# Performance work log

Hardware: AMD Instinct MI355X
Metric: run time of the kernel (lower is better)

The kernel has to match this reference:

```python
import jax, jax.numpy as jnp
import numpy as np

B, T, D = 2, 2048, 1024
N_HEADS, D_HEAD, WINDOW = 16, 64, 256
SCALE = D_HEAD ** -0.5


def setup_inputs() -> dict:
    key = jax.random.key(0)
    k1, k2, k3 = jax.random.split(key, 3)
    x = jax.random.normal(k1, (B, T, D), dtype=jnp.float32)
    # torch Linear weights are [out_features, in_features], init std=0.02
    w_qkv = jax.random.normal(k2, (3 * N_HEADS * D_HEAD, D), dtype=jnp.float32) * 0.02
    w_out = jax.random.normal(k3, (D, N_HEADS * D_HEAD), dtype=jnp.float32) * 0.02
    return {"x": x, "w_qkv": w_qkv, "w_out": w_out}


def reference(x, w_qkv, w_out):
    b, t, d = x.shape
    qkv = jnp.einsum('btd,ed->bte', x, w_qkv)  # [B,T,3*H*Dh]
    q, k, v = jnp.split(qkv, 3, axis=-1)
    def heads(u):
        return u.reshape(b, t, N_HEADS, D_HEAD).transpose(0, 2, 1, 3)  # [B,H,T,Dh]
    q, k, v = heads(q), heads(k), heads(v)
    scores = jnp.einsum('bhqd,bhkd->bhqk', q, k) * SCALE  # [B,H,T,T]
    pos = jnp.arange(t)
    dist = pos[:, None] - pos[None, :]  # query - key
    allowed = (dist >= 0) & (dist < WINDOW)  # causal sliding window
    neg_inf = jnp.asarray(-jnp.inf, dtype=scores.dtype)
    scores = jnp.where(allowed[None, None], scores, neg_inf)
    attn = jax.nn.softmax(scores, axis=-1)
    out = jnp.einsum('bhqk,bhkd->bhqd', attn, v)  # [B,H,T,Dh]
    out = out.transpose(0, 2, 1, 3).reshape(b, t, N_HEADS * D_HEAD)
    return jnp.einsum('bte,de->btd', out, w_out)
```

## Files before the change

kernel.cpp:

```cpp
#include <hip/hip_runtime.h>
#include <hip/hip_bf16.h>

typedef unsigned short bfu;
typedef __attribute__((ext_vector_type(8))) short short8;
typedef __attribute__((ext_vector_type(4))) float floatx4;

#define B_ 2
#define T_ 2048
#define D_ 1024
#define NH 16
#define DH 64
#define WIN 256
#define QKV_COLS 3072
#define NX  (B_ * T_ * D_)
#define NWQ (QKV_COLS * D_)
#define NWO (D_ * D_)

__device__ __forceinline__ bfu f2b_bits(float f) {
  union { __hip_bfloat16 h; bfu u; } cv;
  cv.h = __float2bfloat16(f);
  return cv.u;
}

__device__ __forceinline__ void gl_lds16(const bfu* g, bfu* l) {
  __builtin_amdgcn_global_load_lds(
      (const __attribute__((address_space(1))) unsigned int*)g,
      (__attribute__((address_space(3))) unsigned int*)l, 16, 0, 0);
}

__global__ void cvt3_kernel(const float* __restrict__ x, const float* __restrict__ wq,
                            const float* __restrict__ wo, bfu* __restrict__ out) {
  int i = (blockIdx.x * 256 + threadIdx.x) * 4;
  const float* src;
  int off;
  if (i < NX)            { src = x;  off = 0; }
  else if (i < NX + NWQ) { src = wq; off = NX; }
  else                   { src = wo; off = NX + NWQ; }
  floatx4 v = *(const floatx4*)(src + (i - off));
  out[i + 0] = f2b_bits(v.x);
  out[i + 1] = f2b_bits(v.y);
  out[i + 2] = f2b_bits(v.z);
  out[i + 3] = f2b_bits(v.w);
}

template <bool OUT_BF16, int TN, bool SCALE_Q>
__global__ __launch_bounds__(256) void gemm_bt_kernel(const bfu* __restrict__ A,
                                                      const bfu* __restrict__ Bm,
                                                      void* __restrict__ C,
                                                      int M, int N, int K) {
  constexpr int NJ = TN / 32;
  __shared__ __align__(16) bfu As[128][64];
  __shared__ __align__(16) bfu Bs[TN][64];
  const int tid = threadIdx.x;
  const int wave = tid >> 6, lane = tid & 63;
  const int quad = lane >> 4, cl = lane & 15;
  const int lr = lane >> 3, lg = lane & 7, sg = lg ^ lr;
  const int wm = (wave >> 1) * 64, wn = (wave & 1) * (TN / 2);
  const int m0 = blockIdx.y * 128, n0 = blockIdx.x * TN;

  floatx4 acc[4][NJ] = {};

  for (int k0 = 0; k0 < K; k0 += 64) {
    __syncthreads();
#pragma unroll
    for (int i = 0; i < 4; ++i) {
      const int row = i * 32 + wave * 8;
      gl_lds16(A + (size_t)(m0 + row + lr) * K + k0 + sg * 8, &As[row][0]);
    }
#pragma unroll
    for (int i = 0; i < TN / 32; ++i) {
      const int row = i * 32 + wave * 8;
      gl_lds16(Bm + (size_t)(n0 + row + lr) * K + k0 + sg * 8, &Bs[row][0]);
    }
    __syncthreads();
#pragma unroll
    for (int ks = 0; ks < 2; ++ks) {
      const int gsw = ks * 4 + quad;
      short8 af[4], bfr[NJ];
#pragma unroll
      for (int im = 0; im < 4; ++im)
        af[im] = *(const short8*)(&As[wm + im * 16 + cl][(gsw ^ (cl & 7)) << 3]);
#pragma unroll
      for (int in = 0; in < NJ; ++in)
        bfr[in] = *(const short8*)(&Bs[wn + in * 16 + cl][(gsw ^ (cl & 7)) << 3]);
#pragma unroll
      for (int im = 0; im < 4; ++im)
#pragma unroll
        for (int in = 0; in < NJ; ++in)
          acc[im][in] = __builtin_amdgcn_mfma_f32_16x16x32_bf16(af[im], bfr[in], acc[im][in], 0, 0, 0);
    }
  }
  const float qs = (SCALE_Q && n0 < 1024) ? 0.125f : 1.0f;
#pragma unroll
  for (int im = 0; im < 4; ++im) {
#pragma unroll
    for (int r = 0; r < 4; ++r) {
      const size_t row = (size_t)(m0 + wm + im * 16 + quad * 4 + r);
#pragma unroll
      for (int in = 0; in < NJ; ++in) {
        const size_t idx = row * (size_t)N + (n0 + wn + in * 16 + cl);
        if constexpr (OUT_BF16)
          ((bfu*)C)[idx] = f2b_bits(acc[im][in][r] * qs);
        else
          ((float*)C)[idx] = acc[im][in][r];
      }
    }
  }
}

__global__ __launch_bounds__(256) void swa_kernel(const bfu* __restrict__ qkv,
                                                  bfu* __restrict__ aout) {
  __shared__ __align__(16) bfu Qs[64][64];
  __shared__ __align__(16) bfu Ks[2][64][64];
  __shared__ __align__(16) bfu Vs[2][64][64];
  __shared__ __align__(16) bfu Ps[4][16][72];

  const int qt = blockIdx.x, h = blockIdx.y, b = blockIdx.z;
  const int tid = threadIdx.x, wave = tid >> 6, lane = tid & 63;
  const int quad = lane >> 4, cl = lane & 15;
  const int lr = lane >> 3, lg = lane & 7, sg = lg ^ lr;
  const int q0 = qt * 64;
  const bfu* qb = qkv + (size_t)b * T_ * QKV_COLS + h * DH;
  const bfu* kb = qb + 1024;
  const bfu* vb = qb + 2048;

  const int jt0 = (qt >= 4) ? qt - 4 : 0;
  const int njt = qt - jt0 + 1;

  int vrow[2], vcol[2];
#pragma unroll
  for (int i = 0; i < 2; ++i) {
    const int c = tid + i * 256;
    vrow[i] = c >> 3;
    vcol[i] = (c & 7) * 8;
  }

#pragma unroll
  for (int i = 0; i < 2; ++i) {
    const int row = wave * 16 + i * 8;
    gl_lds16(qb + (size_t)(q0 + row + lr) * QKV_COLS + sg * 8, &Qs[row][0]);
    gl_lds16(kb + (size_t)(jt0 * 64 + row + lr) * QKV_COLS + sg * 8, &Ks[0][row][0]);
  }
  {
    union { short8 v; bfu u[8]; } t0[2];
#pragma unroll
    for (int i = 0; i < 2; ++i)
      t0[i].v = *(const short8*)(vb + (size_t)(jt0 * 64 + vrow[i]) * QKV_COLS + vcol[i]);
#pragma unroll
    for (int i = 0; i < 2; ++i)
#pragma unroll
      for (int e = 0; e < 8; ++e) {
        const int d = vcol[i] + e;
        const int swz = (d & 7) ^ ((d >> 3) & 7);
        Vs[0][d][((((vrow[i] >> 3) ^ swz) & 7) << 3) | (vrow[i] & 7)] = t0[i].u[e];
      }
  }
  __syncthreads();

  float l_r[4] = {0.f, 0.f, 0.f, 0.f};
  floatx4 acc_o[4] = {};

  for (int it = 0; it < njt; ++it) {
    const int cur = it & 1, nxt = cur ^ 1;
    const int k0 = (jt0 + it) * 64;
    const bool pf = (it + 1 < njt);

    union { short8 v; bfu u[8]; } vp[2];
    if (pf) {
      const int kn = k0 + 64;
#pragma unroll
      for (int i = 0; i < 2; ++i) {
        const int row = wave * 16 + i * 8;
        gl_lds16(kb + (size_t)(kn + row + lr) * QKV_COLS + sg * 8, &Ks[nxt][row][0]);
      }
#pragma unroll
      for (int i = 0; i < 2; ++i)
        vp[i].v = *(const short8*)(vb + (size_t)(kn + vrow[i]) * QKV_COLS + vcol[i]);
    }

    floatx4 s[4] = {};
#pragma unroll
    for (int ks = 0; ks < 2; ++ks) {
      const int gsw = ks * 4 + quad;
      short8 aq = *(const short8*)(&Qs[wave * 16 + cl][(gsw ^ (cl & 7)) << 3]);
#pragma unroll
      for (int j = 0; j < 4; ++j) {
        short8 bk = *(const short8*)(&Ks[cur][j * 16 + cl][(gsw ^ (cl & 7)) << 3]);
        s[j] = __builtin_amdgcn_mfma_f32_16x16x32_bf16(aq, bk, s[j], 0, 0, 0);
      }
    }

#pragma unroll
    for (int r = 0; r < 4; ++r) {
      const int qg = q0 + wave * 16 + quad * 4 + r;
      float ssum = 0.f;
#pragma unroll
      for (int j = 0; j < 4; ++j) {
        const int kg = k0 + j * 16 + cl;
        const int dist = qg - kg;
        const float p = (dist >= 0 && dist < WIN) ? __expf(s[j][r]) : 0.f;
        s[j][r] = p;
        ssum += p;
      }
      l_r[r] += ssum;
    }

#pragma unroll
    for (int j = 0; j < 4; ++j)
#pragma unroll
      for (int r = 0; r < 4; ++r)
        Ps[wave][quad * 4 + r][j * 16 + cl] = f2b_bits(s[j][r]);
#pragma unroll
    for (int ks = 0; ks < 2; ++ks) {
      const int kq = ks * 32 + quad * 8;
      short8 ap = *(const short8*)(&Ps[wave][cl][kq]);
#pragma unroll
      for (int j = 0; j < 4; ++j) {
        const int d = j * 16 + cl;
        const int swz = (d & 7) ^ ((d >> 3) & 7);
        short8 bv = *(const short8*)(&Vs[cur][d][(((ks * 4 + quad) ^ swz) & 7) << 3]);
        acc_o[j] = __builtin_amdgcn_mfma_f32_16x16x32_bf16(ap, bv, acc_o[j], 0, 0, 0);
      }
    }

    if (pf) {
#pragma unroll
      for (int i = 0; i < 2; ++i)
#pragma unroll
        for (int e = 0; e < 8; ++e) {
          const int d = vcol[i] + e;
          const int swz = (d & 7) ^ ((d >> 3) & 7);
          Vs[nxt][d][((((vrow[i] >> 3) ^ swz) & 7) << 3) | (vrow[i] & 7)] = vp[i].u[e];
        }
    }
    __syncthreads();
  }

#pragma unroll
  for (int r = 0; r < 4; ++r) {
    float l = l_r[r];
    l += __shfl_xor(l, 1);
    l += __shfl_xor(l, 2);
    l += __shfl_xor(l, 4);
    l += __shfl_xor(l, 8);
    l_r[r] = 1.f / l;
  }
  bfu* ob = aout + (size_t)b * T_ * D_ + h * DH;
#pragma unroll
  for (int r = 0; r < 4; ++r) {
    const size_t row = (size_t)(q0 + wave * 16 + quad * 4 + r);
#pragma unroll
    for (int j = 0; j < 4; ++j)
      ob[row * D_ + j * 16 + cl] = f2b_bits(acc_o[j][r] * l_r[r]);
  }
}

extern "C" void kernel_launch(void* const* d_in, const int* in_sizes, int n_in,
                              void* d_out, int out_size, void* d_ws, size_t ws_size,
                              hipStream_t stream) {
  const float* x     = (const float*)d_in[0];
  const float* w_qkv = (const float*)d_in[1];
  const float* w_out = (const float*)d_in[2];
  float* out = (float*)d_out;
  char* ws = (char*)d_ws;

  bfu* xb    = (bfu*)(ws);
  bfu* wqkvb = (bfu*)(ws + (8ull << 20));
  bfu* woutb = (bfu*)(ws + (14ull << 20));
  bfu* qkvb  = (bfu*)(ws + (16ull << 20));
  bfu* attb  = (bfu*)(ws + (40ull << 20));

  cvt3_kernel<<<(NX + NWQ + NWO) / 1024, 256, 0, stream>>>(x, w_qkv, w_out, xb);

  gemm_bt_kernel<true, 128, true><<<dim3(QKV_COLS / 128, (B_ * T_) / 128), 256, 0, stream>>>(
      xb, wqkvb, qkvb, B_ * T_, QKV_COLS, D_);

  swa_kernel<<<dim3(T_ / 64, NH, B_), 256, 0, stream>>>(qkvb, attb);

  gemm_bt_kernel<false, 64, false><<<dim3(D_ / 64, (B_ * T_) / 128), 256, 0, stream>>>(
      attb, woutb, out, B_ * T_, D_, D_);
}
```

Measured before the change: 152.5 us.

## Keep softmax P in registers by transposing S and using fp16 PV MFMA

The attention kernel now computes S transposed (K as A operand, Q as B), so each lane holds four consecutive keys for one query. Those probabilities are packed straight into fp16 registers as the A operand of a 16x16x16 f16 MFMA, removing the per-wave shared-memory P buffer and its write/read round trip. V is emitted as fp16 by the QKV GEMM epilogue and stored in LDS with a new rotated layout suited to 4-element reads. The row-sum reduction is rewritten for the transposed layout, and the kernel gets a launch_bounds occupancy hint. The trade-offs are twice as many smaller MFMAs and a mix of fp16 V with bf16 Q/K.

```diff
diff --git a/kernel.cpp b/kernel.cpp
--- a/kernel.cpp
+++ b/kernel.cpp
@@ -4,6 +4,8 @@
 typedef unsigned short bfu;
 typedef __attribute__((ext_vector_type(8))) short short8;
 typedef __attribute__((ext_vector_type(4))) float floatx4;
+typedef __attribute__((ext_vector_type(2))) __fp16 fp16x2;
+typedef __attribute__((ext_vector_type(4))) _Float16 half4v;
 
 #define B_ 2
 #define T_ 2048
@@ -43,7 +45,7 @@
   out[i + 3] = f2b_bits(v.w);
 }
 
-template <bool OUT_BF16, int TN, bool SCALE_Q>
+template <int EPI, int TN>
 __global__ __launch_bounds__(256) void gemm_bt_kernel(const bfu* __restrict__ A,
                                                       const bfu* __restrict__ Bm,
                                                       void* __restrict__ C,
@@ -90,7 +92,8 @@
           acc[im][in] = __builtin_amdgcn_mfma_f32_16x16x32_bf16(af[im], bfr[in], acc[im][in], 0, 0, 0);
     }
   }
-  const float qs = (SCALE_Q && n0 < 1024) ? 0.125f : 1.0f;
+  const float qs = (EPI == 2 && n0 < 1024) ? 0.125f : 1.0f;
+  const bool vf16 = (EPI == 2) && (n0 >= 2048);
 #pragma unroll
   for (int im = 0; im < 4; ++im) {
 #pragma unroll
@@ -99,21 +102,25 @@
 #pragma unroll
       for (int in = 0; in < NJ; ++in) {
         const size_t idx = row * (size_t)N + (n0 + wn + in * 16 + cl);
-        if constexpr (OUT_BF16)
-          ((bfu*)C)[idx] = f2b_bits(acc[im][in][r] * qs);
-        else
-          ((float*)C)[idx] = acc[im][in][r];
-      }
-    }
-  }
-}
-
-__global__ __launch_bounds__(256) void swa_kernel(const bfu* __restrict__ qkv,
-                                                  bfu* __restrict__ aout) {
+        const float val = acc[im][in][r];
+        if constexpr (EPI == 0) {
+          ((float*)C)[idx] = val;
+        } else {
+          bfu bits;
+          if (vf16) { union { _Float16 h; bfu u; } cv; cv.h = (_Float16)val; bits = cv.u; }
+          else      { bits = f2b_bits(val * qs); }
+          ((bfu*)C)[idx] = bits;
+        }
+      }
+    }
+  }
+}
+
+__global__ __launch_bounds__(256, 4) void swa_kernel(const bfu* __restrict__ qkv,
+                                                     bfu* __restrict__ aout) {
   __shared__ __align__(16) bfu Qs[64][64];
   __shared__ __align__(16) bfu Ks[2][64][64];
   __shared__ __align__(16) bfu Vs[2][64][64];
-  __shared__ __align__(16) bfu Ps[4][16][72];
 
   const int qt = blockIdx.x, h = blockIdx.y, b = blockIdx.z;
   const int tid = threadIdx.x, wave = tid >> 6, lane = tid & 63;
@@ -150,15 +157,16 @@
     for (int i = 0; i < 2; ++i)
 #pragma unroll
       for (int e = 0; e < 8; ++e) {
-        const int d = vcol[i] + e;
-        const int swz = (d & 7) ^ ((d >> 3) & 7);
-        Vs[0][d][((((vrow[i] >> 3) ^ swz) & 7) << 3) | (vrow[i] & 7)] = t0[i].u[e];
+        const int d = vcol[i] + e, k = vrow[i];
+        const int gp = ((k >> 2) + d + (d >> 3)) & 15;
+        Vs[0][d][gp * 4 + (k & 3)] = t0[i].u[e];
       }
   }
   __syncthreads();
 
-  float l_r[4] = {0.f, 0.f, 0.f, 0.f};
-  floatx4 acc_o[4] = {};
+  float l_acc = 0.f;
+  floatx4 acc[4] = {};
+  const int ddc = cl + (cl >> 3);
 
   for (int it = 0; it < njt; ++it) {
     const int cur = it & 1, nxt = cur ^ 1;
@@ -181,45 +189,41 @@
     floatx4 s[4] = {};
 #pragma unroll
     for (int ks = 0; ks < 2; ++ks) {
-      const int gsw = ks * 4 + quad;
-      short8 aq = *(const short8*)(&Qs[wave * 16 + cl][(gsw ^ (cl & 7)) << 3]);
-#pragma unroll
-      for (int j = 0; j < 4; ++j) {
-        short8 bk = *(const short8*)(&Ks[cur][j * 16 + cl][(gsw ^ (cl & 7)) << 3]);
-        s[j] = __builtin_amdgcn_mfma_f32_16x16x32_bf16(aq, bk, s[j], 0, 0, 0);
-      }
-    }
-
-#pragma unroll
-    for (int r = 0; r < 4; ++r) {
-      const int qg = q0 + wave * 16 + quad * 4 + r;
-      float ssum = 0.f;
-#pragma unroll
-      for (int j = 0; j < 4; ++j) {
-        const int kg = k0 + j * 16 + cl;
+      const int col = ((ks * 4 + quad) ^ (cl & 7)) << 3;
+      short8 bq = *(const short8*)(&Qs[wave * 16 + cl][col]);
+#pragma unroll
+      for (int jk = 0; jk < 4; ++jk) {
+        short8 ak = *(const short8*)(&Ks[cur][jk * 16 + cl][col]);
+        s[jk] = __builtin_amdgcn_mfma_f32_16x16x32_bf16(ak, bq, s[jk], 0, 0, 0);
+      }
+    }
+
+    const int qg = q0 + wave * 16 + cl;
+    half4v af[4];
+#pragma unroll
+    for (int jk = 0; jk < 4; ++jk) {
+      float p[4];
+#pragma unroll
+      for (int r = 0; r < 4; ++r) {
+        const int kg = k0 + jk * 16 + quad * 4 + r;
         const int dist = qg - kg;
-        const float p = (dist >= 0 && dist < WIN) ? __expf(s[j][r]) : 0.f;
-        s[j][r] = p;
-        ssum += p;
-      }
-      l_r[r] += ssum;
-    }
-
-#pragma unroll
-    for (int j = 0; j < 4; ++j)
-#pragma unroll
-      for (int r = 0; r < 4; ++r)
-        Ps[wave][quad * 4 + r][j * 16 + cl] = f2b_bits(s[j][r]);
-#pragma unroll
-    for (int ks = 0; ks < 2; ++ks) {
-      const int kq = ks * 32 + quad * 8;
-      short8 ap = *(const short8*)(&Ps[wave][cl][kq]);
-#pragma unroll
-      for (int j = 0; j < 4; ++j) {
-        const int d = j * 16 + cl;
-        const int swz = (d & 7) ^ ((d >> 3) & 7);
-        short8 bv = *(const short8*)(&Vs[cur][d][(((ks * 4 + quad) ^ swz) & 7) << 3]);
-        acc_o[j] = __builtin_amdgcn_mfma_f32_16x16x32_bf16(ap, bv, acc_o[j], 0, 0, 0);
+        p[r] = (dist >= 0 && dist < WIN) ? __expf(s[jk][r]) : 0.f;
+        l_acc += p[r];
+      }
+      union { fp16x2 h2[2]; half4v h4; } u;
+      u.h2[0] = __builtin_amdgcn_cvt_pkrtz(p[0], p[1]);
+      u.h2[1] = __builtin_amdgcn_cvt_pkrtz(p[2], p[3]);
+      af[jk] = u.h4;
+    }
+
+#pragma unroll
+    for (int kt = 0; kt < 4; ++kt) {
+#pragma unroll
+      for (int jd = 0; jd < 4; ++jd) {
+        const int d = jd * 16 + cl;
+        const int gp = (kt * 4 + quad + ddc + jd * 2) & 15;
+        half4v bv = *(const half4v*)(&Vs[cur][d][gp * 4]);
+        acc[jd] = __builtin_amdgcn_mfma_f32_16x16x16f16(af[kt], bv, acc[jd], 0, 0, 0);
       }
     }
 
@@ -228,30 +232,28 @@
       for (int i = 0; i < 2; ++i)
 #pragma unroll
         for (int e = 0; e < 8; ++e) {
-          const int d = vcol[i] + e;
-          const int swz = (d & 7) ^ ((d >> 3) & 7);
-          Vs[nxt][d][((((vrow[i] >> 3) ^ swz) & 7) << 3) | (vrow[i] & 7)] = vp[i].u[e];
+          const int d = vcol[i] + e, k = vrow[i];
+          const int gp = ((k >> 2) + d + (d >> 3)) & 15;
+          Vs[nxt][d][gp * 4 + (k & 3)] = vp[i].u[e];
         }
     }
     __syncthreads();
   }
 
-#pragma unroll
-  for (int r = 0; r < 4; ++r) {
-    float l = l_r[r];
-    l += __shfl_xor(l, 1);
-    l += __shfl_xor(l, 2);
-    l += __shfl_xor(l, 4);
-    l += __shfl_xor(l, 8);
-    l_r[r] = 1.f / l;
-  }
+  l_acc += __shfl_xor(l_acc, 16);
+  l_acc += __shfl_xor(l_acc, 32);
+  const float linv = 1.f / l_acc;
+  float lq[4];
+#pragma unroll
+  for (int r = 0; r < 4; ++r) lq[r] = __shfl(linv, quad * 4 + r);
+
   bfu* ob = aout + (size_t)b * T_ * D_ + h * DH;
 #pragma unroll
   for (int r = 0; r < 4; ++r) {
     const size_t row = (size_t)(q0 + wave * 16 + quad * 4 + r);
 #pragma unroll
-    for (int j = 0; j < 4; ++j)
-      ob[row * D_ + j * 16 + cl] = f2b_bits(acc_o[j][r] * l_r[r]);
+    for (int jd = 0; jd < 4; ++jd)
+      ob[row * D_ + jd * 16 + cl] = f2b_bits(acc[jd][r] * lq[r]);
   }
 }
 
@@ -272,11 +274,11 @@
 
   cvt3_kernel<<<(NX + NWQ + NWO) / 1024, 256, 0, stream>>>(x, w_qkv, w_out, xb);
 
-  gemm_bt_kernel<true, 128, true><<<dim3(QKV_COLS / 128, (B_ * T_) / 128), 256, 0, stream>>>(
+  gemm_bt_kernel<2, 128><<<dim3(QKV_COLS / 128, (B_ * T_) / 128), 256, 0, stream>>>(
       xb, wqkvb, qkvb, B_ * T_, QKV_COLS, D_);
 
   swa_kernel<<<dim3(T_ / 64, NH, B_), 256, 0, stream>>>(qkvb, attb);
 
-  gemm_bt_kernel<false, 64, false><<<dim3(D_ / 64, (B_ * T_) / 128), 256, 0, stream>>>(
+  gemm_bt_kernel<0, 64><<<dim3(D_ / 64, (B_ * T_) / 128), 256, 0, stream>>>(
       attb, woutb, out, B_ * T_, D_, D_);
 }
```

After: 154.6 us. About the same (+1.4%).
